# Kernel tuning notes

Hardware: AMD Instinct MI355X
Metric: run time of the kernel (lower is better)

The kernel has to match this reference:

```python
import jax, jax.numpy as jnp
import numpy as np

TAU = 2.0
DECAY = float(np.exp(-1.0 / TAU))
THRESH = 1.0  # base_threshold; adaptive update only happens in training mode
LN_EPS = 1e-5
B, S, V, D, L = 16, 256, 32000, 512, 4  # d_state must equal d_model (see shape_source)

@jax.custom_vjp
def atan_spike(x):
    # spikingjelly surrogate.ATan: heaviside fwd, atan surrogate bwd (alpha=2)
    return (x >= 0).astype(x.dtype)

def _atan_fwd(x):
    return atan_spike(x), x

def _atan_bwd(x, g):
    alpha = 2.0
    s = (jnp.pi / 2.0) * alpha * x
    return (g * (alpha / 2.0) / (1.0 + s * s),)

atan_spike.defvjp(_atan_fwd, _atan_bwd)

def lif_step(mem, x):
    mem = mem * DECAY + x
    spike = atan_spike(mem - THRESH)
    mem = mem * (1.0 - jax.lax.stop_gradient(spike))  # reset uses spike.detach()
    return mem, spike

def layer_norm(x, g, b):
    m = jnp.mean(x, axis=-1, keepdims=True)
    v = jnp.mean(jnp.square(x - m), axis=-1, keepdims=True)
    return (x - m) / jnp.sqrt(v + LN_EPS) * g + b

def setup_inputs():
    key = jax.random.key(0)
    ks = jax.random.split(key, 8)
    s = 0.02
    return {
        'input_ids': jax.random.randint(ks[0], (B, S), 0, V),
        'embedding': jax.random.normal(ks[1], (V, D), jnp.float32) * s,
        'enc_W': jax.random.normal(ks[2], (D, D), jnp.float32) * s,
        'enc_b': jnp.zeros((D,), jnp.float32),
        'gen_W': jax.random.normal(ks[3], (L, D, D), jnp.float32) * s,
        'gen_b': jnp.zeros((L, D), jnp.float32),
        'inf_W': jax.random.normal(ks[4], (L, D, D), jnp.float32) * s,
        'inf_b': jnp.zeros((L, D), jnp.float32),
        'err_g': jnp.ones((L, D), jnp.float32),
        'err_b': jnp.zeros((L, D), jnp.float32),
        'st_g': jnp.ones((L, D), jnp.float32),
        'st_b': jnp.zeros((L, D), jnp.float32),
        'out_W': jax.random.normal(ks[5], (V, D), jnp.float32) * s,
        'out_b': jnp.zeros((V,), jnp.float32),
    }

def reference(input_ids, embedding, enc_W, enc_b, gen_W, gen_b, inf_W, inf_b, err_g, err_b, st_g, st_b, out_W, out_b):
    tok = embedding[input_ids]              # [B,S,D]
    xs = jnp.swapaxes(tok, 0, 1)            # [S,B,D] scan over time

    def pc_layer(j, gm, im, bottom_up, top_down):
        # PredictiveCodingLayer.forward (LIF mems gm/im are persistent state)
        gm, pred = lif_step(gm, top_down @ gen_W[j].T + gen_b[j])
        err = layer_norm(jax.nn.relu(bottom_up - pred), err_g[j], err_b[j])
        im, su = lif_step(im, err @ inf_W[j].T + inf_b[j])
        new_state = layer_norm(top_down + su, st_g[j], st_b[j])
        return gm, im, new_state, err, pred

    def step(carry, emb_t):
        enc_mem, gen_mem, inf_mem, states, spk, memp = carry
        enc_mem, bu = lif_step(enc_mem, emb_t @ enc_W.T + enc_b)
        # bottom-up pass
        for j in range(L):
            gm, im, st, err, _ = pc_layer(j, gen_mem[j], inf_mem[j], bu, states[j])
            gen_mem = gen_mem.at[j].set(gm)
            inf_mem = inf_mem.at[j].set(im)
            states = states.at[j].set(st)
            bu = jax.nn.relu(st)
            spk = spk + err.mean()
            memp = memp + jnp.abs(im).mean()
        # top-down generative pass (same layers called again: mems keep evolving)
        td = states[L - 1]
        zb = jnp.zeros_like(bu)
        for j in reversed(range(L)):
            gm, im, _, _, pred = pc_layer(j, gen_mem[j], inf_mem[j], zb, td)
            gen_mem = gen_mem.at[j].set(gm)
            inf_mem = inf_mem.at[j].set(im)
            td = pred
        logits = td @ out_W.T + out_b
        return (enc_mem, gen_mem, inf_mem, states, spk, memp), logits

    init = (jnp.zeros((B, D), jnp.float32), jnp.zeros((L, B, D), jnp.float32),
            jnp.zeros((L, B, D), jnp.float32), jnp.zeros((L, B, D), jnp.float32),
            jnp.float32(0.0), jnp.float32(0.0))
    (_, _, _, _, spk, memp), logits_sb = jax.lax.scan(step, init, xs)
    final_logits = jnp.swapaxes(logits_sb, 0, 1)  # [B,S,V]
    return final_logits, spk / S, memp / S
```

## Files before the change

### kernel.cpp

```cpp
#include <hip/hip_runtime.h>
#include <math.h>

#define S_ 256
#define B_ 16
#define D_ 512
#define V_ 32000
#define L_ 4
#define DEC_ 0.6065306597126334f

typedef short v8s __attribute__((ext_vector_type(8)));
typedef float v4f __attribute__((ext_vector_type(4)));

static __device__ __forceinline__ short f2bf(float f){
  union { float f; unsigned u; } v; v.f = f;
  unsigned r = (v.u + 0x7FFFu + ((v.u >> 16) & 1u)) >> 16;
  return (short)(unsigned short)r;
}

__global__ __launch_bounds__(256) void k_gemm_enc(const int* __restrict__ ids,
                                                  const float* __restrict__ emb,
                                                  const float* __restrict__ encW,
                                                  const float* __restrict__ encb,
                                                  float* __restrict__ X,
                                                  unsigned* __restrict__ counts,
                                                  unsigned* __restrict__ bunz,
                                                  float* __restrict__ accum){
  __shared__ __align__(16) short As[64*40];
  __shared__ __align__(16) short Bs[64*40];
  __shared__ int ids_s[64];
  const int t = threadIdx.x;
  const int bm = blockIdx.x, bn = blockIdx.y;
  if (bn == 0 && bm < 16){
    int g = bm*256 + t;
    counts[g] = 0u;
    bunz[g] = 0u;
    if (g < 2) accum[g] = 0.0f;
  }
  if (t < 64){
    int mg = bm*64 + t;
    int s = mg >> 4, b = mg & 15;
    ids_s[t] = ids[b * S_ + s];
  }
  __syncthreads();
  const int arow = t >> 2;
  const int kc = (t & 3) * 8;
  const int wave = t >> 6;
  const int l = t & 63;
  const int lm = l & 15;
  const int q = l >> 4;
  v4f acc[4] = {};
  for (int k0 = 0; k0 < D_; k0 += 32){
    const float* asrc = emb + (size_t)ids_s[arow] * D_ + k0 + kc;
    float4 a0 = *(const float4*)asrc;
    float4 a1 = *(const float4*)(asrc + 4);
    const float* bsrc = encW + (size_t)(bn*64 + arow) * D_ + k0 + kc;
    float4 b0 = *(const float4*)bsrc;
    float4 b1 = *(const float4*)(bsrc + 4);
    v8s av, bv;
    av[0]=f2bf(a0.x); av[1]=f2bf(a0.y); av[2]=f2bf(a0.z); av[3]=f2bf(a0.w);
    av[4]=f2bf(a1.x); av[5]=f2bf(a1.y); av[6]=f2bf(a1.z); av[7]=f2bf(a1.w);
    bv[0]=f2bf(b0.x); bv[1]=f2bf(b0.y); bv[2]=f2bf(b0.z); bv[3]=f2bf(b0.w);
    bv[4]=f2bf(b1.x); bv[5]=f2bf(b1.y); bv[6]=f2bf(b1.z); bv[7]=f2bf(b1.w);
    *(v8s*)&As[arow*40 + kc] = av;
    *(v8s*)&Bs[arow*40 + kc] = bv;
    __syncthreads();
    v8s af = *(const v8s*)&As[(wave*16 + lm)*40 + q*8];
    #pragma unroll
    for (int n = 0; n < 4; ++n){
      v8s bf = *(const v8s*)&Bs[(n*16 + lm)*40 + q*8];
      acc[n] = __builtin_amdgcn_mfma_f32_16x16x32_bf16(af, bf, acc[n], 0, 0, 0);
    }
    __syncthreads();
  }
  #pragma unroll
  for (int n = 0; n < 4; ++n){
    #pragma unroll
    for (int i = 0; i < 4; ++i){
      int mloc = wave*16 + q*4 + i;
      int nloc = n*16 + lm;
      int r  = bm*64 + mloc;
      int nn = bn*64 + nloc;
      X[(size_t)r * D_ + nn] = acc[n][i] + encb[nn];
    }
  }
}

__global__ __launch_bounds__(64) void k_scan(const float* __restrict__ X,
                                             unsigned char* __restrict__ bu,
                                             unsigned* __restrict__ bunz,
                                             const float* __restrict__ inf_W,
                                             const float* __restrict__ inf_b,
                                             const float* __restrict__ err_b,
                                             float* __restrict__ cvec){
  int bx = blockIdx.x;
  if (bx >= 128){
    int r = bx - 128;
    int j = r >> 3;
    int dp = (r & 7) * 64 + threadIdx.x;
    const float* row = inf_W + ((size_t)j * D_ + dp) * D_;
    const float* eb = err_b + j * D_;
    float acc = inf_b[j * D_ + dp];
    for (int d = 0; d < D_; d += 8){
      float4 w0 = *(const float4*)(row + d);
      float4 w1 = *(const float4*)(row + d + 4);
      float4 e0 = *(const float4*)(eb + d);
      float4 e1 = *(const float4*)(eb + d + 4);
      acc += e0.x*w0.x + e0.y*w0.y + e0.z*w0.z + e0.w*w0.w;
      acc += e1.x*w1.x + e1.y*w1.y + e1.z*w1.z + e1.w*w1.w;
    }
    cvec[j * D_ + dp] = acc;
    return;
  }
  int g = bx * 64 + threadIdx.x;
  int b = g >> 9;
  float mem = 0.0f;
  for (int s0 = 0; s0 < S_; s0 += 8){
    float x[8];
    #pragma unroll
    for (int i = 0; i < 8; ++i) x[i] = X[(size_t)(s0 + i) * (B_*D_) + g];
    #pragma unroll
    for (int i = 0; i < 8; ++i){
      mem = mem * DEC_ + x[i];
      float sp = (mem >= 1.0f) ? 1.0f : 0.0f;
      mem *= (1.0f - sp);
      bu[(size_t)(s0 + i) * (B_*D_) + g] = (unsigned char)sp;
      if (sp != 0.0f) atomicOr(&bunz[(s0 + i) * B_ + b], 1u);
    }
  }
}

__device__ __forceinline__ float wave_sum(float x){
  #pragma unroll
  for (int o = 32; o > 0; o >>= 1) x += __shfl_xor(x, o);
  return x;
}

__device__ void wave_matvec(const float* __restrict__ W, const float* __restrict__ bias,
                            const float x[8], float y[8], float* xs, int l){
  __syncthreads();
  #pragma unroll
  for (int i = 0; i < 8; ++i) xs[l + 64*i] = x[i];
  __syncthreads();
  #pragma unroll
  for (int i = 0; i < 8; ++i){
    int dp = l + 64*i;
    const float* row = W + (size_t)dp * D_;
    float acc = bias[dp];
    for (int d = 0; d < D_; d += 4){
      float4 w = *(const float4*)(row + d);
      acc += xs[d]*w.x + xs[d+1]*w.y + xs[d+2]*w.z + xs[d+3]*w.w;
    }
    y[i] = acc;
  }
}

__device__ void wave_ln(const float e[8], const float* __restrict__ g,
                        const float* __restrict__ bb, float out[8], int l){
  float s = 0.f;
  #pragma unroll
  for (int i = 0; i < 8; ++i) s += e[i];
  float m = wave_sum(s) * (1.0f/512.0f);
  float s2 = 0.f;
  #pragma unroll
  for (int i = 0; i < 8; ++i){ float d = e[i] - m; s2 += d*d; }
  float var = wave_sum(s2) * (1.0f/512.0f);
  float inv = 1.0f / sqrtf(var + 1e-5f);
  #pragma unroll
  for (int i = 0; i < 8; ++i){
    int d = l + 64*i;
    out[i] = (e[i] - m) * inv * g[d] + bb[d];
  }
}

__global__ __launch_bounds__(64) void k_sim(
    const float* __restrict__ gen_W, const float* __restrict__ gen_b,
    const float* __restrict__ inf_W, const float* __restrict__ inf_b,
    const float* __restrict__ err_g, const float* __restrict__ err_b,
    const float* __restrict__ st_g, const float* __restrict__ st_b,
    const unsigned char* __restrict__ bu8, const unsigned* __restrict__ bunz,
    const float* __restrict__ cvec,
    unsigned* __restrict__ counts, unsigned short* __restrict__ idxb,
    float* __restrict__ accum)
{
  const int b = blockIdx.x, l = threadIdx.x;
  __shared__ float xs[D_];
  __shared__ unsigned scnt;
  float st[4][8], gm[4][8], im[4][8];
  #pragma unroll
  for (int j = 0; j < 4; ++j)
    #pragma unroll
    for (int i = 0; i < 8; ++i){ st[j][i]=0.f; gm[j][i]=0.f; im[j][i]=0.f; }

  bool okz = true;
  #pragma unroll
  for (int j = 0; j < 4; ++j)
    #pragma unroll
    for (int i = 0; i < 8; ++i){
      int d = j*512 + l + 64*i;
      okz = okz && (gen_b[d]==0.f) && (inf_b[d]==0.f) && (err_b[d]==0.f) && (st_b[d]==0.f);
    }
  const bool bias_zero = (__all((int)okz) != 0);

  unsigned long long fl[4];
  #pragma unroll
  for (int w = 0; w < 4; ++w){
    unsigned v = bunz[(w*64 + l) * B_ + b];
    fl[w] = __ballot(v != 0u);
  }

  bool state_zero = true;
  float spk_acc = 0.f, memp_acc = 0.f;

  for (int t = 0; t < S_; ++t){
    bool nz = ((fl[t >> 6] >> (t & 63)) & 1ull) != 0ull;
    if (state_zero && bias_zero && !nz) continue;
    state_zero = false;

    float bu[8];
    #pragma unroll
    for (int i = 0; i < 8; ++i) bu[i] = (float)bu8[(size_t)(t*B_ + b)*D_ + l + 64*i];

    #pragma unroll
    for (int j = 0; j < 4; ++j){
      float y[8];
      wave_matvec(gen_W + (size_t)j*D_*D_, gen_b + j*D_, st[j], y, xs, l);
      float pred[8];
      #pragma unroll
      for (int i = 0; i < 8; ++i){
        gm[j][i] = gm[j][i]*DEC_ + y[i];
        pred[i] = (gm[j][i] >= 1.0f) ? 1.0f : 0.0f;
        gm[j][i] *= (1.0f - pred[i]);
      }
      float e[8];
      #pragma unroll
      for (int i = 0; i < 8; ++i){ float v = bu[i] - pred[i]; e[i] = v > 0.f ? v : 0.f; }
      float eo[8];
      wave_ln(e, err_g + j*D_, err_b + j*D_, eo, l);
      #pragma unroll
      for (int i = 0; i < 8; ++i) spk_acc += eo[i];
      float y2[8];
      wave_matvec(inf_W + (size_t)j*D_*D_, inf_b + j*D_, eo, y2, xs, l);
      float su[8];
      #pragma unroll
      for (int i = 0; i < 8; ++i){
        im[j][i] = im[j][i]*DEC_ + y2[i];
        su[i] = (im[j][i] >= 1.0f) ? 1.0f : 0.0f;
        im[j][i] *= (1.0f - su[i]);
        memp_acc += fabsf(im[j][i]);
      }
      float tmp[8];
      #pragma unroll
      for (int i = 0; i < 8; ++i) tmp[i] = st[j][i] + su[i];
      wave_ln(tmp, st_g + j*D_, st_b + j*D_, st[j], l);
      #pragma unroll
      for (int i = 0; i < 8; ++i) bu[i] = st[j][i] > 0.f ? st[j][i] : 0.f;
    }

    float td[8];
    #pragma unroll
    for (int i = 0; i < 8; ++i) td[i] = st[3][i];
    #pragma unroll
    for (int j = 3; j >= 0; --j){
      float y[8];
      wave_matvec(gen_W + (size_t)j*D_*D_, gen_b + j*D_, td, y, xs, l);
      #pragma unroll
      for (int i = 0; i < 8; ++i){
        gm[j][i] = gm[j][i]*DEC_ + y[i];
        float p = (gm[j][i] >= 1.0f) ? 1.0f : 0.0f;
        gm[j][i] *= (1.0f - p);
        td[i] = p;
      }
      #pragma unroll
      for (int i = 0; i < 8; ++i){
        float c = cvec[j*D_ + l + 64*i];
        im[j][i] = im[j][i]*DEC_ + c;
        float ss = (im[j][i] >= 1.0f) ? 1.0f : 0.0f;
        im[j][i] *= (1.0f - ss);
      }
    }

    if (l == 0) scnt = 0u;
    __syncthreads();
    unsigned base = (unsigned)(t*B_ + b) * D_;
    #pragma unroll
    for (int i = 0; i < 8; ++i){
      if (td[i] != 0.f){
        unsigned pos = atomicAdd(&scnt, 1u);
        idxb[base + pos] = (unsigned short)(l + 64*i);
      }
    }
    __syncthreads();
    if (l == 0) counts[t*B_ + b] = scnt;
  }
  spk_acc = wave_sum(spk_acc);
  memp_acc = wave_sum(memp_acc);
  if (l == 0){
    atomicAdd(&accum[0], spk_acc);
    atomicAdd(&accum[1], memp_acc);
  }
}

__global__ __launch_bounds__(64) void k_logits(const unsigned* __restrict__ counts,
                                               const unsigned short* __restrict__ idxb,
                                               const float* __restrict__ outW,
                                               const float* __restrict__ outb,
                                               const float* __restrict__ accum,
                                               float* __restrict__ out){
  const int chunk = blockIdx.x % 25;
  const int rg = blockIdx.x / 25;
  const int lane = threadIdx.x;
  if (blockIdx.x == 0 && lane == 0){
    const float inv = 1.0f / (float)(B_ * D_ * S_);
    out[(size_t)B_ * S_ * V_ + 0] = accum[0] * inv;
    out[(size_t)B_ * S_ * V_ + 1] = accum[1] * inv;
  }
  const int colbase = chunk * 1280;
  v4f pay[5];
  #pragma unroll
  for (int k = 0; k < 5; ++k)
    pay[k] = *(const v4f*)(outb + colbase + k*256 + lane*4);

  int prow = rg*32 + (lane & 31);
  unsigned myc = counts[(prow & 255) * B_ + (prow >> 8)];

  for (int r = 0; r < 32; ++r){
    int row = rg*32 + r;
    unsigned cnt = (unsigned)__shfl((int)myc, r);
    float* dst = out + (size_t)row * V_ + colbase;
    if (cnt == 0){
      #pragma unroll
      for (int k = 0; k < 5; ++k)
        __builtin_nontemporal_store(pay[k], (v4f*)(dst + k*256 + lane*4));
    } else {
      int s = row & 255, b = row >> 8;
      unsigned base = (unsigned)(s * B_ + b) * D_;
      v4f acc[5];
      #pragma unroll
      for (int k = 0; k < 5; ++k) acc[k] = pay[k];
      for (unsigned i = 0; i < cnt; ++i){
        int d = idxb[base + i];
        #pragma unroll
        for (int k = 0; k < 5; ++k){
          int v = colbase + k*256 + lane*4;
          acc[k].x += outW[(size_t)(v+0)*D_ + d];
          acc[k].y += outW[(size_t)(v+1)*D_ + d];
          acc[k].z += outW[(size_t)(v+2)*D_ + d];
          acc[k].w += outW[(size_t)(v+3)*D_ + d];
        }
      }
      #pragma unroll
      for (int k = 0; k < 5; ++k)
        __builtin_nontemporal_store(acc[k], (v4f*)(dst + k*256 + lane*4));
    }
  }
}

extern "C" void kernel_launch(void* const* d_in, const int* in_sizes, int n_in,
                              void* d_out, int out_size, void* d_ws, size_t ws_size,
                              hipStream_t stream){
  (void)in_sizes; (void)n_in; (void)out_size; (void)ws_size;
  const int*   input_ids = (const int*)d_in[0];
  const float* embedding = (const float*)d_in[1];
  const float* enc_W = (const float*)d_in[2];
  const float* enc_b = (const float*)d_in[3];
  const float* gen_W = (const float*)d_in[4];
  const float* gen_b = (const float*)d_in[5];
  const float* inf_W = (const float*)d_in[6];
  const float* inf_b = (const float*)d_in[7];
  const float* err_g = (const float*)d_in[8];
  const float* err_b = (const float*)d_in[9];
  const float* st_g  = (const float*)d_in[10];
  const float* st_b  = (const float*)d_in[11];
  const float* out_W = (const float*)d_in[12];
  const float* out_b = (const float*)d_in[13];
  float* out = (float*)d_out;
  char* ws = (char*)d_ws;

  float*          X      = (float*)(ws + 0);
  unsigned char*  bu     = (unsigned char*)(ws + 8388608);
  unsigned short* idxb   = (unsigned short*)(ws + 10485760);
  unsigned*       counts = (unsigned*)(ws + 14680064);
  unsigned*       bunz   = (unsigned*)(ws + 14696448);
  float*          cvec   = (float*)(ws + 14712832);
  float*          accum  = (float*)(ws + 14721024);

  hipLaunchKernelGGL(k_gemm_enc, dim3(64, 8), dim3(256), 0, stream,
                     input_ids, embedding, enc_W, enc_b, X, counts, bunz, accum);
  hipLaunchKernelGGL(k_scan, dim3(160), dim3(64), 0, stream,
                     X, bu, bunz, inf_W, inf_b, err_b, cvec);
  hipLaunchKernelGGL(k_sim, dim3(16), dim3(64), 0, stream,
                     gen_W, gen_b, inf_W, inf_b, err_g, err_b, st_g, st_b,
                     bu, bunz, cvec, counts, idxb, accum);
  hipLaunchKernelGGL(k_logits, dim3(3200), dim3(64), 0, stream,
                     counts, idxb, out_W, out_b, accum, out);
}
```

Measured before the change: 704.4 us.

## Move cvec precompute into encoder GEMM, use bf16 intrinsics, pair logits rows

```diff
diff --git a/kernel.cpp b/kernel.cpp
--- a/kernel.cpp
+++ b/kernel.cpp
@@ -1,4 +1,5 @@
 #include <hip/hip_runtime.h>
+#include <hip/hip_bf16.h>
 #include <math.h>
 
 #define S_ 256
@@ -10,12 +11,6 @@
 
 typedef short v8s __attribute__((ext_vector_type(8)));
 typedef float v4f __attribute__((ext_vector_type(4)));
-
-static __device__ __forceinline__ short f2bf(float f){
-  union { float f; unsigned u; } v; v.f = f;
-  unsigned r = (v.u + 0x7FFFu + ((v.u >> 16) & 1u)) >> 16;
-  return (short)(unsigned short)r;
-}
 
 __global__ __launch_bounds__(256) void k_gemm_enc(const int* __restrict__ ids,
                                                   const float* __restrict__ emb,
@@ -24,12 +19,37 @@
                                                   float* __restrict__ X,
                                                   unsigned* __restrict__ counts,
                                                   unsigned* __restrict__ bunz,
-                                                  float* __restrict__ accum){
+                                                  float* __restrict__ accum,
+                                                  const float* __restrict__ inf_W,
+                                                  const float* __restrict__ inf_b,
+                                                  const float* __restrict__ err_b,
+                                                  float* __restrict__ cvec){
+  const int t = threadIdx.x;
+  const int bm = blockIdx.x, bn = blockIdx.y;
+  if (bm == 64){
+    if (bn >= 4) return;
+    int j = bn;
+    #pragma unroll
+    for (int h = 0; h < 2; ++h){
+      int dp = t + h*256;
+      const float* row = inf_W + ((size_t)j * D_ + dp) * D_;
+      const float* eb = err_b + j * D_;
+      float acc = inf_b[j * D_ + dp];
+      for (int d = 0; d < D_; d += 8){
+        float4 w0 = *(const float4*)(row + d);
+        float4 w1 = *(const float4*)(row + d + 4);
+        float4 e0 = *(const float4*)(eb + d);
+        float4 e1 = *(const float4*)(eb + d + 4);
+        acc += e0.x*w0.x + e0.y*w0.y + e0.z*w0.z + e0.w*w0.w;
+        acc += e1.x*w1.x + e1.y*w1.y + e1.z*w1.z + e1.w*w1.w;
+      }
+      cvec[j * D_ + dp] = acc;
+    }
+    return;
+  }
   __shared__ __align__(16) short As[64*40];
   __shared__ __align__(16) short Bs[64*40];
   __shared__ int ids_s[64];
-  const int t = threadIdx.x;
-  const int bm = blockIdx.x, bn = blockIdx.y;
   if (bn == 0 && bm < 16){
     int g = bm*256 + t;
     counts[g] = 0u;
@@ -56,13 +76,17 @@
     const float* bsrc = encW + (size_t)(bn*64 + arow) * D_ + k0 + kc;
     float4 b0 = *(const float4*)bsrc;
     float4 b1 = *(const float4*)(bsrc + 4);
-    v8s av, bv;
-    av[0]=f2bf(a0.x); av[1]=f2bf(a0.y); av[2]=f2bf(a0.z); av[3]=f2bf(a0.w);
-    av[4]=f2bf(a1.x); av[5]=f2bf(a1.y); av[6]=f2bf(a1.z); av[7]=f2bf(a1.w);
-    bv[0]=f2bf(b0.x); bv[1]=f2bf(b0.y); bv[2]=f2bf(b0.z); bv[3]=f2bf(b0.w);
-    bv[4]=f2bf(b1.x); bv[5]=f2bf(b1.y); bv[6]=f2bf(b1.z); bv[7]=f2bf(b1.w);
-    *(v8s*)&As[arow*40 + kc] = av;
-    *(v8s*)&Bs[arow*40 + kc] = bv;
+    union { v8s v; __hip_bfloat162 h[4]; } ua, ub;
+    ua.h[0] = __float22bfloat162_rn(make_float2(a0.x, a0.y));
+    ua.h[1] = __float22bfloat162_rn(make_float2(a0.z, a0.w));
+    ua.h[2] = __float22bfloat162_rn(make_float2(a1.x, a1.y));
+    ua.h[3] = __float22bfloat162_rn(make_float2(a1.z, a1.w));
+    ub.h[0] = __float22bfloat162_rn(make_float2(b0.x, b0.y));
+    ub.h[1] = __float22bfloat162_rn(make_float2(b0.z, b0.w));
+    ub.h[2] = __float22bfloat162_rn(make_float2(b1.x, b1.y));
+    ub.h[3] = __float22bfloat162_rn(make_float2(b1.z, b1.w));
+    *(v8s*)&As[arow*40 + kc] = ua.v;
+    *(v8s*)&Bs[arow*40 + kc] = ub.v;
     __syncthreads();
     v8s af = *(const v8s*)&As[(wave*16 + lm)*40 + q*8];
     #pragma unroll
@@ -87,39 +111,16 @@
 
 __global__ __launch_bounds__(64) void k_scan(const float* __restrict__ X,
                                              unsigned char* __restrict__ bu,
-                                             unsigned* __restrict__ bunz,
-                                             const float* __restrict__ inf_W,
-                                             const float* __restrict__ inf_b,
-                                             const float* __restrict__ err_b,
-                                             float* __restrict__ cvec){
-  int bx = blockIdx.x;
-  if (bx >= 128){
-    int r = bx - 128;
-    int j = r >> 3;
-    int dp = (r & 7) * 64 + threadIdx.x;
-    const float* row = inf_W + ((size_t)j * D_ + dp) * D_;
-    const float* eb = err_b + j * D_;
-    float acc = inf_b[j * D_ + dp];
-    for (int d = 0; d < D_; d += 8){
-      float4 w0 = *(const float4*)(row + d);
-      float4 w1 = *(const float4*)(row + d + 4);
-      float4 e0 = *(const float4*)(eb + d);
-      float4 e1 = *(const float4*)(eb + d + 4);
-      acc += e0.x*w0.x + e0.y*w0.y + e0.z*w0.z + e0.w*w0.w;
-      acc += e1.x*w1.x + e1.y*w1.y + e1.z*w1.z + e1.w*w1.w;
-    }
-    cvec[j * D_ + dp] = acc;
-    return;
-  }
-  int g = bx * 64 + threadIdx.x;
+                                             unsigned* __restrict__ bunz){
+  int g = blockIdx.x * 64 + threadIdx.x;
   int b = g >> 9;
   float mem = 0.0f;
-  for (int s0 = 0; s0 < S_; s0 += 8){
-    float x[8];
-    #pragma unroll
-    for (int i = 0; i < 8; ++i) x[i] = X[(size_t)(s0 + i) * (B_*D_) + g];
-    #pragma unroll
-    for (int i = 0; i < 8; ++i){
+  for (int s0 = 0; s0 < S_; s0 += 16){
+    float x[16];
+    #pragma unroll
+    for (int i = 0; i < 16; ++i) x[i] = X[(size_t)(s0 + i) * (B_*D_) + g];
+    #pragma unroll
+    for (int i = 0; i < 16; ++i){
       mem = mem * DEC_ + x[i];
       float sp = (mem >= 1.0f) ? 1.0f : 0.0f;
       mem *= (1.0f - sp);
@@ -300,6 +301,31 @@
   }
 }
 
+__device__ __forceinline__ void logits_general(float* __restrict__ dst, const v4f pay[5],
+                                               const unsigned short* __restrict__ idxb,
+                                               const float* __restrict__ outW,
+                                               int row, int colbase, int lane, unsigned cnt){
+  int s = row & 255, b = row >> 8;
+  unsigned base = (unsigned)(s * B_ + b) * D_;
+  v4f acc[5];
+  #pragma unroll
+  for (int k = 0; k < 5; ++k) acc[k] = pay[k];
+  for (unsigned i = 0; i < cnt; ++i){
+    int d = idxb[base + i];
+    #pragma unroll
+    for (int k = 0; k < 5; ++k){
+      int v = colbase + k*256 + lane*4;
+      acc[k].x += outW[(size_t)(v+0)*D_ + d];
+      acc[k].y += outW[(size_t)(v+1)*D_ + d];
+      acc[k].z += outW[(size_t)(v+2)*D_ + d];
+      acc[k].w += outW[(size_t)(v+3)*D_ + d];
+    }
+  }
+  #pragma unroll
+  for (int k = 0; k < 5; ++k)
+    __builtin_nontemporal_store(acc[k], (v4f*)(dst + k*256 + lane*4));
+}
+
 __global__ __launch_bounds__(64) void k_logits(const unsigned* __restrict__ counts,
                                                const unsigned short* __restrict__ idxb,
                                                const float* __restrict__ outW,
@@ -323,34 +349,21 @@
   int prow = rg*32 + (lane & 31);
   unsigned myc = counts[(prow & 255) * B_ + (prow >> 8)];
 
-  for (int r = 0; r < 32; ++r){
-    int row = rg*32 + r;
-    unsigned cnt = (unsigned)__shfl((int)myc, r);
-    float* dst = out + (size_t)row * V_ + colbase;
-    if (cnt == 0){
-      #pragma unroll
-      for (int k = 0; k < 5; ++k)
-        __builtin_nontemporal_store(pay[k], (v4f*)(dst + k*256 + lane*4));
+  for (int r = 0; r < 32; r += 2){
+    int row0 = rg*32 + r, row1 = row0 + 1;
+    unsigned c0 = (unsigned)__shfl((int)myc, r);
+    unsigned c1 = (unsigned)__shfl((int)myc, r + 1);
+    float* dst0 = out + (size_t)row0 * V_ + colbase;
+    float* dst1 = out + (size_t)row1 * V_ + colbase;
+    if ((c0 | c1) == 0u){
+      #pragma unroll
+      for (int k = 0; k < 5; ++k){
+        __builtin_nontemporal_store(pay[k], (v4f*)(dst0 + k*256 + lane*4));
+        __builtin_nontemporal_store(pay[k], (v4f*)(dst1 + k*256 + lane*4));
+      }
     } else {
-      int s = row & 255, b = row >> 8;
-      unsigned base = (unsigned)(s * B_ + b) * D_;
-      v4f acc[5];
-      #pragma unroll
-      for (int k = 0; k < 5; ++k) acc[k] = pay[k];
-      for (unsigned i = 0; i < cnt; ++i){
-        int d = idxb[base + i];
-        #pragma unroll
-        for (int k = 0; k < 5; ++k){
-          int v = colbase + k*256 + lane*4;
-          acc[k].x += outW[(size_t)(v+0)*D_ + d];
-          acc[k].y += outW[(size_t)(v+1)*D_ + d];
-          acc[k].z += outW[(size_t)(v+2)*D_ + d];
-          acc[k].w += outW[(size_t)(v+3)*D_ + d];
-        }
-      }
-      #pragma unroll
-      for (int k = 0; k < 5; ++k)
-        __builtin_nontemporal_store(acc[k], (v4f*)(dst + k*256 + lane*4));
+      logits_general(dst0, pay, idxb, outW, row0, colbase, lane, c0);
+      logits_general(dst1, pay, idxb, outW, row1, colbase, lane, c1);
     }
   }
 }
@@ -384,10 +397,10 @@
   float*          cvec   = (float*)(ws + 14712832);
   float*          accum  = (float*)(ws + 14721024);
 
-  hipLaunchKernelGGL(k_gemm_enc, dim3(64, 8), dim3(256), 0, stream,
-                     input_ids, embedding, enc_W, enc_b, X, counts, bunz, accum);
-  hipLaunchKernelGGL(k_scan, dim3(160), dim3(64), 0, stream,
-                     X, bu, bunz, inf_W, inf_b, err_b, cvec);
+  hipLaunchKernelGGL(k_gemm_enc, dim3(65, 8), dim3(256), 0, stream,
+                     input_ids, embedding, enc_W, enc_b, X, counts, bunz, accum,
+                     inf_W, inf_b, err_b, cvec);
+  hipLaunchKernelGGL(k_scan, dim3(128), dim3(64), 0, stream, X, bu, bunz);
   hipLaunchKernelGGL(k_sim, dim3(16), dim3(64), 0, stream,
                      gen_W, gen_b, inf_W, inf_b, err_g, err_b, st_g, st_b,
                      bu, bunz, cvec, counts, idxb, accum);
```

After: 723.7 us. 2.7% more time.
